# Performance work log

Hardware: AMD Instinct MI355X
Metric: run time of the kernel (lower is better)

## Reference

```python
import jax, jax.numpy as jnp
import numpy as np

E = 8        # number of sessions (experts)
N = 512      # per-session input width (max units)
P = 512      # n_channels (output width)
F = 100      # max_F time bins
B = 128      # batch of trials
SCALE = 1.0


def setup_inputs() -> dict:
    key = jax.random.key(0)
    kx, ke, k1, k2, k3, k4 = jax.random.split(key, 6)
    x = jax.random.normal(kx, (B, F, N), dtype=jnp.float32)
    eid = jax.random.randint(ke, (B,), 0, E, dtype=jnp.int32)
    # Per-session stitcher Linear(N, 2N) and projector Linear(2N, P), stacked.
    s1 = 1.0 / np.sqrt(N)
    s2 = 1.0 / np.sqrt(2 * N)
    W1 = jax.random.uniform(k1, (E, N, 2 * N), jnp.float32, -s1, s1)
    b1 = jax.random.uniform(k2, (E, 2 * N), jnp.float32, -s1, s1)
    W2 = jax.random.uniform(k3, (E, 2 * N, P), jnp.float32, -s2, s2)
    b2 = jax.random.uniform(k4, (E, P), jnp.float32, -s2, s2)
    return {"x": x, "eid": eid, "W1": W1, "b1": b1, "W2": W2, "b2": b2}


def reference(x, eid, W1, b1, W2, b2):
    # Grouped (per-session) Linear -> Softsign -> Linear, dispatched by eid.
    # Equivalent to the torch loop over unique eids with mask gather/scatter,
    # expressed as a gather of per-sample expert weights + batched matmul.
    w1 = W1[eid]                      # [B, N, 2N]
    stitched = jnp.einsum('bfn,bnh->bfh', x, w1) + b1[eid][:, None, :]
    act = stitched / (1.0 + jnp.abs(stitched))  # Softsign
    act = act * SCALE
    w2 = W2[eid]                      # [B, 2N, P]
    out = jnp.einsum('bfh,bhp->bfp', act, w2) + b2[eid][:, None, :]
    return out                        # [B, F, P]
```

## Files before the change

### kernel.cpp

```cpp
#include <hip/hip_runtime.h>
#include <hip/hip_bf16.h>

#define B_ 128
#define F_ 100
#define N_ 512
#define H_ 1024
#define P_ 512
#define E_ 8
#define BK 64
#define AROWS 112

typedef __attribute__((ext_vector_type(8))) short bf16x8;
typedef __attribute__((ext_vector_type(4))) float f32x4;

#define GLOAD16(g, l) __builtin_amdgcn_global_load_lds(                      \
    (const __attribute__((address_space(1))) void*)(g),                      \
    (__attribute__((address_space(3))) void*)(l), 16, 0, 0)

static __device__ __forceinline__ short f2bf(float f) {
    __hip_bfloat16 h = __float2bfloat16(f);
    short s;
    __builtin_memcpy(&s, &h, sizeof(s));
    return s;
}

__global__ __launch_bounds__(256) void prep(
    const float* __restrict__ x, const float* __restrict__ W1,
    const float* __restrict__ W2, const int* __restrict__ eid,
    short* __restrict__ xbf, short* __restrict__ W1T, short* __restrict__ W2T,
    int2* __restrict__ ttab) {
    __shared__ float tile[64][65];
    __shared__ int scnt[E_], sbase[E_];
    const int bx = blockIdx.x;
    const int t = threadIdx.x;
    if (bx < 3200) {
        const int g = bx * 256 + t;
        const int col = (g & 63) * 8;
        const int row = g >> 6;
        const float* xp = x + (size_t)row * N_ + col;
        const float4 v0 = *(const float4*)(xp);
        const float4 v1 = *(const float4*)(xp + 4);
        union { short s[8]; uint4 u; } o;
        o.s[0] = f2bf(v0.x); o.s[1] = f2bf(v0.y);
        o.s[2] = f2bf(v0.z); o.s[3] = f2bf(v0.w);
        o.s[4] = f2bf(v1.x); o.s[5] = f2bf(v1.y);
        o.s[6] = f2bf(v1.z); o.s[7] = f2bf(v1.w);
        *(uint4*)(xbf + (size_t)row * N_ + col) = o.u;
    } else if (bx < 5248) {
        const float* W; short* WT; int R, C, r0, c0, e;
        if (bx < 4224) {
            const int idx = bx - 3200;
            e = idx >> 7; const int i = idx & 127;
            W = W1; WT = W1T; R = N_; C = H_;
            r0 = (i >> 4) * 64; c0 = (i & 15) * 64;
        } else {
            const int idx = bx - 4224;
            e = idx >> 7; const int i = idx & 127;
            W = W2; WT = W2T; R = H_; C = P_;
            r0 = (i & 15) * 64; c0 = (i >> 4) * 64;
        }
        const float* Wp = W + (size_t)e * R * C;
        short* WTp = WT + (size_t)e * C * R;
        {
            const int c4 = (t & 15) * 4, r = t >> 4;
#pragma unroll
            for (int p = 0; p < 4; p++) {
                const int row = p * 16 + r;
                const float4 v = *(const float4*)(Wp + (size_t)(r0 + row) * C + c0 + c4);
                tile[row][c4 + 0] = v.x; tile[row][c4 + 1] = v.y;
                tile[row][c4 + 2] = v.z; tile[row][c4 + 3] = v.w;
            }
        }
        __syncthreads();
        {
            const int r8 = (t & 7) * 8, cl = t >> 3;
#pragma unroll
            for (int p = 0; p < 2; p++) {
                const int c = p * 32 + cl;
                union { short s[8]; uint4 u; } o;
#pragma unroll
                for (int j = 0; j < 8; j++) o.s[j] = f2bf(tile[r8 + j][c]);
                *(uint4*)(&WTp[(size_t)(c0 + c) * R + r0 + r8]) = o.u;
            }
        }
    } else {
        if (t < E_) scnt[t] = 0;
        __syncthreads();
        int my_e = 0;
        if (t < B_) { my_e = eid[t]; atomicAdd(&scnt[my_e], 1); }
        __syncthreads();
        if (t == 0) {
            int s = 0;
            for (int i = 0; i < E_; i++) { sbase[i] = s; s += scnt[i]; }
        }
        __syncthreads();
        if (t < B_) {
            const int pos = atomicAdd(&sbase[my_e], 1);
            ttab[pos] = make_int2(t, my_e);
        }
    }
}

template <int KDIM, int BN_, bool FIRST, int MINW, bool DBUF>
__global__ __launch_bounds__(256, MINW) void gemm_kernel(
    const short* __restrict__ A,
    const short* __restrict__ WT,
    const float* __restrict__ bias,
    const int2* __restrict__ ttab,
    short* __restrict__ actout,
    float* __restrict__ out)
{
    constexpr int NCOLS = FIRST ? H_ : P_;
    constexpr int NI = BN_ / 32;
    constexpr int STAGE1 = (AROWS + BN_) * BK;
    constexpr int NBUF = DBUF ? 2 : 1;
    constexpr int EPI_SH = 4 * 4096;
    constexpr int SBUF_SH = (STAGE1 * NBUF > EPI_SH) ? STAGE1 * NBUF : EPI_SH;
    __shared__ short sbuf[SBUF_SH];
    const int slot = (blockIdx.x & 7) * 16 + (blockIdx.x >> 3);
    const int2 te = ttab[slot];
    const int trial = te.x, e = te.y;
    const int n0 = blockIdx.y * BN_;
    const int t = threadIdx.x;
    const int lane = t & 63, w = t >> 6;
    const int wm = (w >> 1) * 64, wn = (w & 1) * (BN_ / 2);
    const int l15 = lane & 15, quad = lane >> 4;
    const int lr = lane >> 3;
    const int lc = (((lane & 7) ^ lr) * 8);

    f32x4 acc[4][NI];
#pragma unroll
    for (int mi = 0; mi < 4; mi++)
#pragma unroll
        for (int ni = 0; ni < NI; ni++)
            acc[mi][ni] = (f32x4)(0.0f);

    float bv[NI];
#pragma unroll
    for (int ni = 0; ni < NI; ni++)
        bv[ni] = bias[(size_t)e * NCOLS + n0 + wn + ni * 16 + l15];

    const short* Ap = A + (size_t)trial * F_ * KDIM;
    const short* Bp = WT + ((size_t)e * NCOLS + n0) * KDIM;

    auto stage = [&](int k0, short* sbase) {
        short* sA = sbase;
        short* sB = sbase + AROWS * BK;
#pragma unroll
        for (int i = 0; i < 4; i++) {
            const int rb = w * 32 + i * 8;
            if (rb < AROWS)
                GLOAD16(Ap + (size_t)(rb + lr) * KDIM + k0 + lc, &sA[rb * BK]);
        }
#pragma unroll
        for (int i = 0; i < NI; i++) {
            const int rb = w * (BN_ / 4) + i * 8;
            GLOAD16(Bp + (size_t)(rb + lr) * KDIM + k0 + lc, &sB[rb * BK]);
        }
    };

    auto compute = [&](const short* sbase) {
        const short* sA = sbase;
        const short* sB = sbase + AROWS * BK;
#pragma unroll
        for (int ks = 0; ks < 2; ks++) {
            const int sw = (((ks * 4 + quad) ^ (l15 & 7)) * 8);
            bf16x8 af, bfr[NI];
#pragma unroll
            for (int ni = 0; ni < NI; ni++)
                bfr[ni] = *(const bf16x8*)(&sB[(wn + ni * 16 + l15) * BK + sw]);
#pragma unroll
            for (int mi = 0; mi < 4; mi++) {
                if (wm + mi * 16 < F_) {
                    af = *(const bf16x8*)(&sA[(wm + mi * 16 + l15) * BK + sw]);
#pragma unroll
                    for (int ni = 0; ni < NI; ni++)
                        acc[mi][ni] = __builtin_amdgcn_mfma_f32_16x16x32_bf16(af, bfr[ni], acc[mi][ni], 0, 0, 0);
                }
            }
        }
    };

    if constexpr (DBUF) {
        short* b0 = sbuf;
        short* b1 = sbuf + STAGE1;
        stage(0, b0);
        __syncthreads();
        for (int k0 = 0; k0 < KDIM; k0 += 2 * BK) {
            stage(k0 + BK, b1);
            compute(b0);
            __syncthreads();
            if (k0 + 2 * BK < KDIM) stage(k0 + 2 * BK, b0);
            compute(b1);
            __syncthreads();
        }
    } else {
        for (int k0 = 0; k0 < KDIM; k0 += BK) {
            stage(k0, sbuf);
            __syncthreads();
            compute(sbuf);
            __syncthreads();
        }
    }

    if constexpr (FIRST) {
        short* sW = sbuf + w * 4096;
#pragma unroll
        for (int mi = 0; mi < 4; mi++) {
#pragma unroll
            for (int ni = 0; ni < 4; ni++) {
                const int cl = ni * 16 + l15;
#pragma unroll
                for (int r = 0; r < 4; r++) {
                    const int rl = mi * 16 + quad * 4 + r;
                    float v = acc[mi][ni][r] + bv[ni];
                    v = v / (1.0f + fabsf(v));
                    sW[rl * 64 + (((cl >> 3) ^ (rl & 7)) * 8) + (cl & 7)] = f2bf(v);
                }
            }
        }
#pragma unroll
        for (int i = 0; i < 8; i++) {
            const int rl = i * 8 + lr;
            const int c = lane & 7;
            const bf16x8 v = *(const bf16x8*)(&sW[rl * 64 + ((c ^ lr) * 8)]);
            const int grow = wm + rl;
            if (grow < F_)
                *(bf16x8*)(&actout[((size_t)trial * F_ + grow) * H_ + n0 + wn + c * 8]) = v;
        }
    } else {
        float* fW = (float*)(sbuf) + w * 2048;
#pragma unroll
        for (int pass = 0; pass < NI; pass += 2) {
#pragma unroll
            for (int mi = 0; mi < 4; mi++) {
#pragma unroll
                for (int nj = 0; nj < 2; nj++) {
                    const int cl = nj * 16 + l15;
#pragma unroll
                    for (int r = 0; r < 4; r++) {
                        const int rl = mi * 16 + quad * 4 + r;
                        fW[rl * 32 + (((cl >> 2) ^ (rl & 7)) * 4) + (cl & 3)] =
                            acc[mi][pass + nj][r] + bv[pass + nj];
                    }
                }
            }
#pragma unroll
            for (int i = 0; i < 8; i++) {
                const int rl = i * 8 + lr;
                const int c = lane & 7;
                const float4 v = *(const float4*)(&fW[rl * 32 + ((c ^ lr) * 4)]);
                const int grow = wm + rl;
                if (grow < F_)
                    *(float4*)(&out[((size_t)trial * F_ + grow) * P_ + n0 + wn + pass * 16 + c * 4]) = v;
            }
        }
    }
}

extern "C" void kernel_launch(void* const* d_in, const int* in_sizes, int n_in,
                              void* d_out, int out_size, void* d_ws, size_t ws_size,
                              hipStream_t stream) {
    const float* x  = (const float*)d_in[0];
    const int* eid  = (const int*)d_in[1];
    const float* W1 = (const float*)d_in[2];
    const float* b1 = (const float*)d_in[3];
    const float* W2 = (const float*)d_in[4];
    const float* b2 = (const float*)d_in[5];
    float* out = (float*)d_out;

    char* ws = (char*)d_ws;
    short* W1T = (short*)(ws);
    short* W2T = (short*)(ws + (size_t)(8u << 20));
    short* act = (short*)(ws + (size_t)(16u << 20));
    short* xbf = (short*)(ws + (size_t)(43u << 20));
    int2* ttab = (int2*)(ws + (size_t)(57u << 20));

    prep<<<dim3(5249), 256, 0, stream>>>(x, W1, W2, eid, xbf, W1T, W2T, ttab);
    gemm_kernel<N_, 128, true, 4, false><<<dim3(B_, H_ / 128), 256, 0, stream>>>(xbf, W1T, b1, ttab, act, nullptr);
    gemm_kernel<H_, 128, false, 2, true><<<dim3(B_, P_ / 128), 256, 0, stream>>>(act, W2T, b2, ttab, nullptr, out);
}
```

Measured before the change: 152.5 us.

## Use double-buffered pipeline with partial vmcnt waits for both GEMMs

Both GEMM kernels now use a double-buffered LDS pipeline that issues the next tile's direct-to-LDS loads before waiting only on the previous tile's loads (per-wave vmcnt counts), then barriers. The first GEMM previously used a single buffer with full syncthreads and 4 waves/EU occupancy; it now uses two buffers and launch bounds of 2. The intent is to overlap global loads with MFMA compute. It risks lower occupancy for the first GEMM, and it depends on exact hand-coded vmcnt counts, which break if the load count per wave changes.

```diff
diff --git a/kernel.cpp b/kernel.cpp
--- a/kernel.cpp
+++ b/kernel.cpp
@@ -101,8 +101,8 @@
     }
 }
 
-template <int KDIM, int BN_, bool FIRST, int MINW, bool DBUF>
-__global__ __launch_bounds__(256, MINW) void gemm_kernel(
+template <int KDIM, int BN_, bool FIRST>
+__global__ __launch_bounds__(256, 2) void gemm_kernel(
     const short* __restrict__ A,
     const short* __restrict__ WT,
     const float* __restrict__ bias,
@@ -113,9 +113,8 @@
     constexpr int NCOLS = FIRST ? H_ : P_;
     constexpr int NI = BN_ / 32;
     constexpr int STAGE1 = (AROWS + BN_) * BK;
-    constexpr int NBUF = DBUF ? 2 : 1;
     constexpr int EPI_SH = 4 * 4096;
-    constexpr int SBUF_SH = (STAGE1 * NBUF > EPI_SH) ? STAGE1 * NBUF : EPI_SH;
+    constexpr int SBUF_SH = (2 * STAGE1 > EPI_SH) ? 2 * STAGE1 : EPI_SH;
     __shared__ short sbuf[SBUF_SH];
     const int slot = (blockIdx.x & 7) * 16 + (blockIdx.x >> 3);
     const int2 te = ttab[slot];
@@ -143,9 +142,9 @@
     const short* Ap = A + (size_t)trial * F_ * KDIM;
     const short* Bp = WT + ((size_t)e * NCOLS + n0) * KDIM;
 
-    auto stage = [&](int k0, short* sbase) {
-        short* sA = sbase;
-        short* sB = sbase + AROWS * BK;
+    auto stage = [&](int k0, short* sb) {
+        short* sA = sb;
+        short* sB = sb + AROWS * BK;
 #pragma unroll
         for (int i = 0; i < 4; i++) {
             const int rb = w * 32 + i * 8;
@@ -159,9 +158,9 @@
         }
     };
 
-    auto compute = [&](const short* sbase) {
-        const short* sA = sbase;
-        const short* sB = sbase + AROWS * BK;
+    auto compute = [&](const short* sb) {
+        const short* sA = sb;
+        const short* sB = sb + AROWS * BK;
 #pragma unroll
         for (int ks = 0; ks < 2; ks++) {
             const int sw = (((ks * 4 + quad) ^ (l15 & 7)) * 8);
@@ -181,27 +180,41 @@
         }
     };
 
-    if constexpr (DBUF) {
-        short* b0 = sbuf;
-        short* b1 = sbuf + STAGE1;
-        stage(0, b0);
-        __syncthreads();
-        for (int k0 = 0; k0 < KDIM; k0 += 2 * BK) {
-            stage(k0 + BK, b1);
-            compute(b0);
-            __syncthreads();
-            if (k0 + 2 * BK < KDIM) stage(k0 + 2 * BK, b0);
-            compute(b1);
-            __syncthreads();
-        }
-    } else {
-        for (int k0 = 0; k0 < KDIM; k0 += BK) {
-            stage(k0, sbuf);
-            __syncthreads();
-            compute(sbuf);
-            __syncthreads();
-        }
+    auto wait_prev_and_bar = [&]() {
+        if (w < 3) asm volatile("s_waitcnt vmcnt(8)" ::: "memory");
+        else       asm volatile("s_waitcnt vmcnt(6)" ::: "memory");
+        __builtin_amdgcn_s_barrier();
+        __builtin_amdgcn_sched_barrier(0);
+    };
+    auto bar = [&]() {
+        __builtin_amdgcn_sched_barrier(0);
+        __builtin_amdgcn_s_barrier();
+        __builtin_amdgcn_sched_barrier(0);
+    };
+
+    short* b0 = sbuf;
+    short* b1 = sbuf + STAGE1;
+
+    stage(0, b0);
+    for (int k0 = 0; k0 < KDIM - 2 * BK; k0 += 2 * BK) {
+        stage(k0 + BK, b1);
+        wait_prev_and_bar();
+        compute(b0);
+        bar();
+        stage(k0 + 2 * BK, b0);
+        wait_prev_and_bar();
+        compute(b1);
+        bar();
     }
+    stage(KDIM - BK, b1);
+    wait_prev_and_bar();
+    compute(b0);
+    bar();
+    asm volatile("s_waitcnt vmcnt(0)" ::: "memory");
+    __builtin_amdgcn_s_barrier();
+    __builtin_amdgcn_sched_barrier(0);
+    compute(b1);
+    bar();
 
     if constexpr (FIRST) {
         short* sW = sbuf + w * 4096;
@@ -277,6 +290,6 @@
     int2* ttab = (int2*)(ws + (size_t)(57u << 20));
 
     prep<<<dim3(5249), 256, 0, stream>>>(x, W1, W2, eid, xbf, W1T, W2T, ttab);
-    gemm_kernel<N_, 128, true, 4, false><<<dim3(B_, H_ / 128), 256, 0, stream>>>(xbf, W1T, b1, ttab, act, nullptr);
-    gemm_kernel<H_, 128, false, 2, true><<<dim3(B_, P_ / 128), 256, 0, stream>>>(act, W2T, b2, ttab, nullptr, out);
-}
+    gemm_kernel<N_, 128, true><<<dim3(B_, H_ / 128), 256, 0, stream>>>(xbf, W1T, b1, ttab, act, nullptr);
+    gemm_kernel<H_, 128, false><<<dim3(B_, P_ / 128), 256, 0, stream>>>(act, W2T, b2, ttab, nullptr, out);
+}
```

Result: no change. 151.2 us (-0.8%).

## Pair two expert-sorted trials per block to share weight tiles in LDS

Applied to the files above, without the earlier changes.

Each 512-thread block now processes two consecutive trials from the expert-sorted table. When both trials use the same expert, the weight tile is loaded into LDS once and read by both 256-thread halves, which cuts global weight traffic. The second GEMM gives up double buffering for a single-stage loop with two barriers per K step, and the two halves run the epilogue one after the other because they share LDS. This trades load latency hiding and some serialization for weight reuse and fewer blocks.

```diff
diff --git a/kernel.cpp b/kernel.cpp
--- a/kernel.cpp
+++ b/kernel.cpp
@@ -101,8 +101,8 @@
     }
 }
 
-template <int KDIM, int BN_, bool FIRST, int MINW, bool DBUF>
-__global__ __launch_bounds__(256, MINW) void gemm_kernel(
+template <int KDIM, bool FIRST>
+__global__ __launch_bounds__(512, 4) void gemm_pair(
     const short* __restrict__ A,
     const short* __restrict__ WT,
     const float* __restrict__ bias,
@@ -111,23 +111,25 @@
     float* __restrict__ out)
 {
     constexpr int NCOLS = FIRST ? H_ : P_;
-    constexpr int NI = BN_ / 32;
-    constexpr int STAGE1 = (AROWS + BN_) * BK;
-    constexpr int NBUF = DBUF ? 2 : 1;
-    constexpr int EPI_SH = 4 * 4096;
-    constexpr int SBUF_SH = (STAGE1 * NBUF > EPI_SH) ? STAGE1 * NBUF : EPI_SH;
-    __shared__ short sbuf[SBUF_SH];
-    const int slot = (blockIdx.x & 7) * 16 + (blockIdx.x >> 3);
-    const int2 te = ttab[slot];
-    const int trial = te.x, e = te.y;
-    const int n0 = blockIdx.y * BN_;
+    constexpr int BN = 128, NI = 4;
+    __shared__ short sbuf[2 * AROWS * BK + 2 * BN * BK];
+    const int pair = (blockIdx.x & 7) * 8 + (blockIdx.x >> 3);
+    const int2 te0 = ttab[2 * pair], te1 = ttab[2 * pair + 1];
+    const int n0 = blockIdx.y * BN;
     const int t = threadIdx.x;
     const int lane = t & 63, w = t >> 6;
-    const int wm = (w >> 1) * 64, wn = (w & 1) * (BN_ / 2);
+    const int g = w >> 2, wsub = w & 3;
+    const int trial = g ? te1.x : te0.x;
+    const int e     = g ? te1.y : te0.y;
+    const bool dual = (te0.y != te1.y);
+    const int wm = (wsub >> 1) * 64, wn = (wsub & 1) * 64;
     const int l15 = lane & 15, quad = lane >> 4;
     const int lr = lane >> 3;
     const int lc = (((lane & 7) ^ lr) * 8);
 
+    short* sA = sbuf + g * (AROWS * BK);
+    short* sB = sbuf + 2 * (AROWS * BK) + ((dual && g) ? BN * BK : 0);
+
     f32x4 acc[4][NI];
 #pragma unroll
     for (int mi = 0; mi < 4; mi++)
@@ -143,25 +145,21 @@
     const short* Ap = A + (size_t)trial * F_ * KDIM;
     const short* Bp = WT + ((size_t)e * NCOLS + n0) * KDIM;
 
-    auto stage = [&](int k0, short* sbase) {
-        short* sA = sbase;
-        short* sB = sbase + AROWS * BK;
+    for (int k0 = 0; k0 < KDIM; k0 += BK) {
 #pragma unroll
         for (int i = 0; i < 4; i++) {
-            const int rb = w * 32 + i * 8;
+            const int rb = wsub * 32 + i * 8;
             if (rb < AROWS)
                 GLOAD16(Ap + (size_t)(rb + lr) * KDIM + k0 + lc, &sA[rb * BK]);
         }
-#pragma unroll
-        for (int i = 0; i < NI; i++) {
-            const int rb = w * (BN_ / 4) + i * 8;
-            GLOAD16(Bp + (size_t)(rb + lr) * KDIM + k0 + lc, &sB[rb * BK]);
-        }
-    };
-
-    auto compute = [&](const short* sbase) {
-        const short* sA = sbase;
-        const short* sB = sbase + AROWS * BK;
+        if (g == 0 || dual) {
+#pragma unroll
+            for (int i = 0; i < 4; i++) {
+                const int rb = wsub * 32 + i * 8;
+                GLOAD16(Bp + (size_t)(rb + lr) * KDIM + k0 + lc, &sB[rb * BK]);
+            }
+        }
+        __syncthreads();
 #pragma unroll
         for (int ks = 0; ks < 2; ks++) {
             const int sw = (((ks * 4 + quad) ^ (l15 & 7)) * 8);
@@ -179,69 +177,23 @@
                 }
             }
         }
-    };
-
-    if constexpr (DBUF) {
-        short* b0 = sbuf;
-        short* b1 = sbuf + STAGE1;
-        stage(0, b0);
-        __syncthreads();
-        for (int k0 = 0; k0 < KDIM; k0 += 2 * BK) {
-            stage(k0 + BK, b1);
-            compute(b0);
-            __syncthreads();
-            if (k0 + 2 * BK < KDIM) stage(k0 + 2 * BK, b0);
-            compute(b1);
-            __syncthreads();
-        }
-    } else {
-        for (int k0 = 0; k0 < KDIM; k0 += BK) {
-            stage(k0, sbuf);
-            __syncthreads();
-            compute(sbuf);
-            __syncthreads();
-        }
+        __syncthreads();
     }
 
-    if constexpr (FIRST) {
-        short* sW = sbuf + w * 4096;
-#pragma unroll
-        for (int mi = 0; mi < 4; mi++) {
-#pragma unroll
-            for (int ni = 0; ni < 4; ni++) {
-                const int cl = ni * 16 + l15;
-#pragma unroll
-                for (int r = 0; r < 4; r++) {
-                    const int rl = mi * 16 + quad * 4 + r;
-                    float v = acc[mi][ni][r] + bv[ni];
-                    v = v / (1.0f + fabsf(v));
-                    sW[rl * 64 + (((cl >> 3) ^ (rl & 7)) * 8) + (cl & 7)] = f2bf(v);
-                }
-            }
-        }
-#pragma unroll
-        for (int i = 0; i < 8; i++) {
-            const int rl = i * 8 + lr;
-            const int c = lane & 7;
-            const bf16x8 v = *(const bf16x8*)(&sW[rl * 64 + ((c ^ lr) * 8)]);
-            const int grow = wm + rl;
-            if (grow < F_)
-                *(bf16x8*)(&actout[((size_t)trial * F_ + grow) * H_ + n0 + wn + c * 8]) = v;
-        }
-    } else {
-        float* fW = (float*)(sbuf) + w * 2048;
-#pragma unroll
-        for (int pass = 0; pass < NI; pass += 2) {
+    auto epi = [&]() {
+        if constexpr (FIRST) {
+            short* sW = sbuf + wsub * 4096;
 #pragma unroll
             for (int mi = 0; mi < 4; mi++) {
 #pragma unroll
-                for (int nj = 0; nj < 2; nj++) {
-                    const int cl = nj * 16 + l15;
+                for (int ni = 0; ni < 4; ni++) {
+                    const int cl = ni * 16 + l15;
 #pragma unroll
                     for (int r = 0; r < 4; r++) {
                         const int rl = mi * 16 + quad * 4 + r;
-                        fW[rl * 32 + (((cl >> 2) ^ (rl & 7)) * 4) + (cl & 3)] =
-                            acc[mi][pass + nj][r] + bv[pass + nj];
+                        float v = acc[mi][ni][r] + bv[ni];
+                        v = v / (1.0f + fabsf(v));
+                        sW[rl * 64 + (((cl >> 3) ^ (rl & 7)) * 8) + (cl & 7)] = f2bf(v);
                     }
                 }
             }
@@ -249,13 +201,43 @@
             for (int i = 0; i < 8; i++) {
                 const int rl = i * 8 + lr;
                 const int c = lane & 7;
-                const float4 v = *(const float4*)(&fW[rl * 32 + ((c ^ lr) * 4)]);
+                const bf16x8 v = *(const bf16x8*)(&sW[rl * 64 + ((c ^ lr) * 8)]);
                 const int grow = wm + rl;
                 if (grow < F_)
-                    *(float4*)(&out[((size_t)trial * F_ + grow) * P_ + n0 + wn + pass * 16 + c * 4]) = v;
-            }
-        }
-    }
+                    *(bf16x8*)(&actout[((size_t)trial * F_ + grow) * H_ + n0 + wn + c * 8]) = v;
+            }
+        } else {
+            float* fW = (float*)(sbuf) + wsub * 2048;
+#pragma unroll
+            for (int pass = 0; pass < NI; pass += 2) {
+#pragma unroll
+                for (int mi = 0; mi < 4; mi++) {
+#pragma unroll
+                    for (int nj = 0; nj < 2; nj++) {
+                        const int cl = nj * 16 + l15;
+#pragma unroll
+                        for (int r = 0; r < 4; r++) {
+                            const int rl = mi * 16 + quad * 4 + r;
+                            fW[rl * 32 + (((cl >> 2) ^ (rl & 7)) * 4) + (cl & 3)] =
+                                acc[mi][pass + nj][r] + bv[pass + nj];
+                        }
+                    }
+                }
+#pragma unroll
+                for (int i = 0; i < 8; i++) {
+                    const int rl = i * 8 + lr;
+                    const int c = lane & 7;
+                    const float4 v = *(const float4*)(&fW[rl * 32 + ((c ^ lr) * 4)]);
+                    const int grow = wm + rl;
+                    if (grow < F_)
+                        *(float4*)(&out[((size_t)trial * F_ + grow) * P_ + n0 + wn + pass * 16 + c * 4]) = v;
+                }
+            }
+        }
+    };
+    if (g == 0) epi();
+    __syncthreads();
+    if (g == 1) epi();
 }
 
 extern "C" void kernel_launch(void* const* d_in, const int* in_sizes, int n_in,
@@ -277,6 +259,6 @@
     int2* ttab = (int2*)(ws + (size_t)(57u << 20));
 
     prep<<<dim3(5249), 256, 0, stream>>>(x, W1, W2, eid, xbf, W1T, W2T, ttab);
-    gemm_kernel<N_, 128, true, 4, false><<<dim3(B_, H_ / 128), 256, 0, stream>>>(xbf, W1T, b1, ttab, act, nullptr);
-    gemm_kernel<H_, 128, false, 2, true><<<dim3(B_, P_ / 128), 256, 0, stream>>>(act, W2T, b2, ttab, nullptr, out);
-}
+    gemm_pair<N_, true><<<dim3(64, H_ / 128), 512, 0, stream>>>(xbf, W1T, b1, ttab, act, nullptr);
+    gemm_pair<H_, false><<<dim3(64, P_ / 128), 512, 0, stream>>>(act, W2T, b2, ttab, nullptr, out);
+}
```

Result: slower. 165.4 us (+8.5%).
